# Performance work log

Measured on AMD Instinct MI355X. Metric: run time of the kernel, lower is better.

## Reference

```python
import jax, jax.numpy as jnp
import numpy as np

EPS = 1e-5
NUM_GROUPS = 32
MIN_POINTS = 4

def group_norm(x, gamma, beta):
    # x: [N, C]; torch GroupNorm applied on (1, C, N): normalize each group over (C/G, N)
    N, C = x.shape
    xg = x.reshape(N, NUM_GROUPS, C // NUM_GROUPS)
    mean = jnp.mean(xg, axis=(0, 2), keepdims=True)
    var = jnp.mean((xg - mean) ** 2, axis=(0, 2), keepdims=True)
    xn = (xg - mean) * jax.lax.rsqrt(var + EPS)
    return xn.reshape(N, C) * gamma + beta

def setup_inputs() -> dict:
    key = jax.random.key(0)
    ks = jax.random.split(key, 12)
    N, V = 1000000, 100000
    C0, C = 3, 64  # input feats (minus barycentric col), hidden width
    distributed = jax.random.normal(ks[0], (N, C0 + 1), dtype=jnp.float32)
    indices = jax.random.randint(ks[1], (N,), 0, V, dtype=jnp.int32)
    # kaiming_normal fan_in, relu: std = sqrt(2 / fan_in)
    W0 = jax.random.normal(ks[2], (C, C0), dtype=jnp.float32) * np.sqrt(2.0 / C0)
    W1 = jax.random.normal(ks[3], (C, C), dtype=jnp.float32) * np.sqrt(2.0 / C)
    W2 = jax.random.normal(ks[4], (C, C), dtype=jnp.float32) * np.sqrt(2.0 / C)
    b2 = jnp.zeros((C,), dtype=jnp.float32)
    g0 = jnp.ones((C,), dtype=jnp.float32)
    beta0 = jnp.zeros((C,), dtype=jnp.float32)
    g1 = jnp.ones((C,), dtype=jnp.float32)
    beta1 = jnp.zeros((C,), dtype=jnp.float32)
    return {"distributed": distributed, "indices": indices, "num_vertices": V,
            "W0": W0, "W1": W1, "W2": W2, "b2": b2,
            "g0": g0, "beta0": beta0, "g1": g1, "beta1": beta1}

def reference(distributed, indices, num_vertices, W0, W1, W2, b2, g0, beta0, g1, beta1):
    N = distributed.shape[0]
    V = int(num_vertices)
    bary = distributed[:, -1]            # [N]
    x = distributed[:, :-1]              # [N, C0]
    # layer 0: linear (no bias) -> GN -> relu
    x = jax.nn.relu(group_norm(x @ W0.T, g0, beta0))
    # layer 1: linear (no bias) -> GN -> relu
    x = jax.nn.relu(group_norm(x @ W1.T, g1, beta1))
    # layer 2 (last): linear with bias -> relu (no norm)
    x = jax.nn.relu(x @ W2.T + b2)       # [N, C]
    idx = jnp.maximum(indices.astype(jnp.int32), 0)
    # scatter-max pooling into lattice vertices
    seg_max = jax.ops.segment_max(x, idx, num_segments=V)          # [V, C], -inf for empty
    seg_max = jnp.where(jnp.isneginf(seg_max), 0.0, seg_max)
    counts = jax.ops.segment_sum(jnp.ones((N,), x.dtype), idx, num_segments=V)  # [V]
    # argmax recovery: first point index attaining the per-segment max, per channel
    gathered_max = seg_max[idx]                                    # [N, C]
    cand = jnp.where(x == gathered_max, jnp.arange(N, dtype=jnp.int32)[:, None], N)
    argmax = jax.ops.segment_min(cand, idx, num_segments=V)        # [V, C]
    argmax = jnp.minimum(argmax, N - 1)
    bary_reduced = bary[argmax]                                    # [V, C]
    out = jnp.concatenate([seg_max, bary_reduced], axis=1)         # [V, 2C]
    few = (counts < MIN_POINTS)[:, None]
    return jnp.where(few, 0.0, out)
```

## Files before the change

kernel.cpp:

```cpp
#include <hip/hip_runtime.h>
#include <hip/hip_bf16.h>
#include <math.h>

#define MIN_POINTS 4

#define WS_W0P   0
#define WS_B0P   768
#define WS_W1P   1024
#define WS_B1P   17408
#define WS_CNT   17920
#define WS_P0    417920
#define WS_P1    548992
#define NPART    1024
#define TS       68

__global__ void k_stats0(const float4* __restrict__ d4, const int* __restrict__ idx,
                         double* __restrict__ partial0, int* __restrict__ cnt, int N){
  __shared__ double red[4][16];
  int tid = blockIdx.x*blockDim.x + threadIdx.x;
  int stride = gridDim.x*blockDim.x;
  double a[9] = {0,0,0,0,0,0,0,0,0};
  for (int i = tid; i < N; i += stride){
    float4 d = d4[i];
    double x0 = d.x, x1 = d.y, x2 = d.z;
    a[0] += x0; a[1] += x1; a[2] += x2;
    a[3] = fma(x0,x0,a[3]); a[4] = fma(x0,x1,a[4]); a[5] = fma(x0,x2,a[5]);
    a[6] = fma(x1,x1,a[6]); a[7] = fma(x1,x2,a[7]); a[8] = fma(x2,x2,a[8]);
    int v = idx[i]; if (v < 0) v = 0;
    atomicAdd(&cnt[v], 1);
  }
  int lane = threadIdx.x & 63, wid = threadIdx.x >> 6;
  #pragma unroll
  for (int j = 0; j < 9; j++){
    double v = a[j];
    for (int o = 32; o > 0; o >>= 1) v += __shfl_down(v, o, 64);
    if (lane == 0) red[wid][j] = v;
  }
  __syncthreads();
  if (threadIdx.x < 9){
    double s = red[0][threadIdx.x] + red[1][threadIdx.x]
             + red[2][threadIdx.x] + red[3][threadIdx.x];
    partial0[blockIdx.x*16 + threadIdx.x] = s;
  }
}

__global__ void k_fold0(const double* __restrict__ partial0, const float* __restrict__ W0,
                        const float* __restrict__ g0, const float* __restrict__ bt0,
                        float* __restrict__ w0p, float* __restrict__ b0p, int N, int nparts){
  __shared__ double sred[16];
  int t = threadIdx.x, lane = t & 63, g = t >> 6;
  if (g < 9){
    double s = 0.0;
    for (int b = lane; b < nparts; b += 64) s += partial0[b*16 + g];
    for (int o = 32; o > 0; o >>= 1) s += __shfl_down(s, o, 64);
    if (lane == 0) sred[g] = s;
  }
  __syncthreads();
  if (t < 64){
    int c = t;
    double sx0 = sred[0], sx1 = sred[1], sx2 = sred[2];
    double G00 = sred[3], G01 = sred[4], G02 = sred[5], G11 = sred[6], G12 = sred[7], G22 = sred[8];
    double s[2], q[2];
    int chans[2] = { c, c ^ 1 };
    #pragma unroll
    for (int u = 0; u < 2; u++){
      int ch = chans[u];
      double w0 = W0[ch*3+0], w1 = W0[ch*3+1], w2 = W0[ch*3+2];
      s[u] = w0*sx0 + w1*sx1 + w2*sx2;
      q[u] = w0*w0*G00 + w1*w1*G11 + w2*w2*G22 + 2.0*(w0*w1*G01 + w0*w2*G02 + w1*w2*G12);
    }
    double inv  = 1.0 / (2.0 * (double)N);
    double mean = (s[0] + s[1]) * inv;
    double var  = (q[0] + q[1]) * inv - mean*mean;
    double aa   = (1.0 / sqrt(var + 1e-5)) * (double)g0[c];
    b0p[c] = (float)((double)bt0[c] - mean * aa);
    w0p[c]       = (float)((double)W0[c*3+0] * aa);
    w0p[64 + c]  = (float)((double)W0[c*3+1] * aa);
    w0p[128 + c] = (float)((double)W0[c*3+2] * aa);
  }
}

__global__ __launch_bounds__(256, 4)
void k_stats1(const float4* __restrict__ d4,
              const float* __restrict__ w0p, const float* __restrict__ b0p,
              const float* __restrict__ W1, double* __restrict__ part1,
              int N, int ntiles){
  __shared__ float stage[64][TS];
  __shared__ double red[4][128];
  int lane = threadIdx.x & 63;
  int wid  = __builtin_amdgcn_readfirstlane((int)(threadIdx.x >> 6));
  int cbase = wid * 16;
  float w1r[64];
  #pragma unroll
  for (int k = 0; k < 64; k += 4){
    float4 t = *(const float4*)&W1[lane*64 + k];
    w1r[k]=t.x; w1r[k+1]=t.y; w1r[k+2]=t.z; w1r[k+3]=t.w;
  }
  double s0 = 0.0, s1 = 0.0;
  for (int t = blockIdx.x; t < ntiles; t += gridDim.x){
    int rb = t * 64;
    int row = rb + lane;
    float4 d = (row < N) ? d4[row] : make_float4(0.f,0.f,0.f,0.f);
    #pragma unroll
    for (int g = 0; g < 4; g++){
      int c = cbase + g*4;
      float4 h;
      h.x = fmaxf(fmaf(w0p[128+c+0], d.z, fmaf(w0p[64+c+0], d.y, fmaf(w0p[c+0], d.x, b0p[c+0]))), 0.f);
      h.y = fmaxf(fmaf(w0p[128+c+1], d.z, fmaf(w0p[64+c+1], d.y, fmaf(w0p[c+1], d.x, b0p[c+1]))), 0.f);
      h.z = fmaxf(fmaf(w0p[128+c+2], d.z, fmaf(w0p[64+c+2], d.y, fmaf(w0p[c+2], d.x, b0p[c+2]))), 0.f);
      h.w = fmaxf(fmaf(w0p[128+c+3], d.z, fmaf(w0p[64+c+3], d.y, fmaf(w0p[c+3], d.x, b0p[c+3]))), 0.f);
      *(float4*)&stage[lane][c] = h;
    }
    __syncthreads();
    #pragma unroll 2
    for (int rr = 0; rr < 16; rr++){
      int r = cbase + rr;
      float a0 = 0.f, a1 = 0.f, a2 = 0.f, a3 = 0.f;
      #pragma unroll
      for (int kb = 0; kb < 16; kb++){
        float4 h = *(const float4*)&stage[r][kb*4];
        a0 = fmaf(w1r[kb*4+0], h.x, a0);
        a1 = fmaf(w1r[kb*4+1], h.y, a1);
        a2 = fmaf(w1r[kb*4+2], h.z, a2);
        a3 = fmaf(w1r[kb*4+3], h.w, a3);
      }
      if (rb + r < N){
        double y = (double)((a0 + a1) + (a2 + a3));
        s0 += y;
        s1 = fma(y, y, s1);
      }
    }
    __syncthreads();
  }
  red[wid][lane]      = s0;
  red[wid][64 + lane] = s1;
  __syncthreads();
  if (threadIdx.x < 128){
    int t = threadIdx.x;
    part1[blockIdx.x*128 + t] = red[0][t] + red[1][t] + red[2][t] + red[3][t];
  }
}

__global__ void k_fold1(const double* __restrict__ part1, const float* __restrict__ W1,
                        const float* __restrict__ g1, const float* __restrict__ bt1,
                        float* __restrict__ w1p, float* __restrict__ b1p, int N, int nparts){
  __shared__ double sst[128];
  int t = threadIdx.x;
  int s = t >> 3, j = t & 7;
  double acc = 0.0;
  for (int b = j; b < nparts; b += 8) acc += part1[b*128 + s];
  acc += __shfl_down(acc, 4, 8);
  acc += __shfl_down(acc, 2, 8);
  acc += __shfl_down(acc, 1, 8);
  if (j == 0) sst[s] = acc;
  __syncthreads();
  if (t < 64){
    int c = t, p = c ^ 1;
    double inv  = 1.0 / (2.0 * (double)N);
    double mean = (sst[c] + sst[p]) * inv;
    double Ey2  = (sst[64+c] + sst[64+p]) * inv;
    double var  = Ey2 - mean*mean;
    double a    = (1.0 / sqrt(var + 1e-5)) * (double)g1[c];
    b1p[c] = (float)((double)bt1[c] - mean * a);
    for (int k = 0; k < 64; k++)
      w1p[c*64 + k] = (float)((double)W1[c*64 + k] * a);
  }
}

__global__ __launch_bounds__(64, 2)
void k_main(const float4* __restrict__ d4, const int* __restrict__ idx,
            const float* __restrict__ w0p, const float* __restrict__ b0p,
            const float* __restrict__ w1p, const float* __restrict__ b1p,
            const float* __restrict__ W2,  const float* __restrict__ b2,
            unsigned long long* __restrict__ seg, int N, int ntiles){
  __shared__ float xch[64][65];
  int lane = threadIdx.x;
  for (int t = blockIdx.x; t < ntiles; t += gridDim.x){
    int rb  = t * 64;
    int row = rb + lane;
    float4 d = (row < N) ? d4[row] : make_float4(0.f,0.f,0.f,0.f);
    int myv = 0;
    if (row < N){ int v = idx[row]; myv = (v < 0) ? 0 : v; }
    float h0[64];
    #pragma unroll
    for (int c = 0; c < 64; c++){
      float t0 = fmaf(w0p[128+c], d.z, fmaf(w0p[64+c], d.y, fmaf(w0p[c], d.x, b0p[c])));
      h0[c] = fmaxf(t0, 0.f);
    }
    for (int c = 0; c < 64; c++){
      const float* wr = &w1p[c*64];
      float a0 = b1p[c], a1 = 0.f, a2 = 0.f, a3 = 0.f;
      #pragma unroll
      for (int k = 0; k < 64; k += 4){
        a0 = fmaf(wr[k+0], h0[k+0], a0);
        a1 = fmaf(wr[k+1], h0[k+1], a1);
        a2 = fmaf(wr[k+2], h0[k+2], a2);
        a3 = fmaf(wr[k+3], h0[k+3], a3);
      }
      xch[lane][c] = fmaxf((a0 + a1) + (a2 + a3), 0.f);
    }
    __syncthreads();
    float h1[64];
    #pragma unroll
    for (int k = 0; k < 64; k++) h1[k] = xch[lane][k];
    __syncthreads();
    for (int c = 0; c < 64; c++){
      const float* wr = &W2[c*64];
      float a0 = b2[c], a1 = 0.f, a2 = 0.f, a3 = 0.f;
      #pragma unroll
      for (int k = 0; k < 64; k += 4){
        a0 = fmaf(wr[k+0], h1[k+0], a0);
        a1 = fmaf(wr[k+1], h1[k+1], a1);
        a2 = fmaf(wr[k+2], h1[k+2], a2);
        a3 = fmaf(wr[k+3], h1[k+3], a3);
      }
      xch[lane][c] = fmaxf((a0 + a1) + (a2 + a3), 0.f);
    }
    __syncthreads();
    int rmax = min(64, N - rb);
    for (int r = 0; r < rmax; r++){
      float y = xch[r][lane];
      int v = __builtin_amdgcn_readlane(myv, r);
      unsigned int bits = __float_as_uint(y) & 0x7fffffffu;
      unsigned long long packed = ((unsigned long long)bits << 32)
          | (unsigned long long)(unsigned int)(~(unsigned int)(rb + r));
      atomicMax(&seg[(size_t)v*64 + lane], packed);
    }
    __syncthreads();
  }
}

__global__ void k_out(const float4* __restrict__ d4, const int* __restrict__ cnt,
                      float* __restrict__ out, int N, int V){
  int lane = threadIdx.x & 63;
  int w = (int)((blockIdx.x*blockDim.x + threadIdx.x) >> 6);
  if (w >= V) return;
  const unsigned long long* seg = (const unsigned long long*)out;
  unsigned long long p = seg[(size_t)w*64 + lane];
  int c = cnt[w];
  unsigned int bits = (unsigned int)(p >> 32);
  unsigned int rowu = ~(unsigned int)p;
  unsigned int nm1 = (unsigned int)(N - 1);
  if (rowu > nm1) rowu = nm1;
  float val  = __uint_as_float(bits);
  float bary = d4[rowu].w;
  bool few = (c < MIN_POINTS);
  float o0 = few ? 0.f : val;
  float o1 = few ? 0.f : bary;
  out[(size_t)w*128 + lane]      = o0;
  out[(size_t)w*128 + 64 + lane] = o1;
}

extern "C" void kernel_launch(void* const* d_in, const int* in_sizes, int n_in,
                              void* d_out, int out_size, void* d_ws, size_t ws_size,
                              hipStream_t stream) {
  const float4* d4  = (const float4*)d_in[0];
  const int*    idx = (const int*)d_in[1];
  const float*  W0  = (const float*)d_in[3];
  const float*  W1  = (const float*)d_in[4];
  const float*  W2  = (const float*)d_in[5];
  const float*  b2  = (const float*)d_in[6];
  const float*  g0  = (const float*)d_in[7];
  const float*  bt0 = (const float*)d_in[8];
  const float*  g1  = (const float*)d_in[9];
  const float*  bt1 = (const float*)d_in[10];

  int N = in_sizes[0] / 4;
  int V = out_size / 128;
  int ntiles = (N + 63) / 64;

  char* ws = (char*)d_ws;
  float*  w0p = (float*)(ws + WS_W0P);
  float*  b0p = (float*)(ws + WS_B0P);
  float*  w1p = (float*)(ws + WS_W1P);
  float*  b1p = (float*)(ws + WS_B1P);
  int*    cnt = (int*)(ws + WS_CNT);
  double* p0  = (double*)(ws + WS_P0);
  double* p1  = (double*)(ws + WS_P1);

  hipMemsetAsync(cnt, 0, (size_t)V * sizeof(int), stream);
  hipMemsetAsync(d_out, 0, (size_t)out_size * sizeof(float), stream);

  k_stats0<<<NPART, 256, 0, stream>>>(d4, idx, p0, cnt, N);
  k_fold0 <<<1, 1024, 0, stream>>>(p0, W0, g0, bt0, w0p, b0p, N, NPART);
  k_stats1<<<NPART, 256, 0, stream>>>(d4, w0p, b0p, W1, p1, N, ntiles);
  k_fold1 <<<1, 1024, 0, stream>>>(p1, W1, g1, bt1, w1p, b1p, N, NPART);
  k_main  <<<2048, 64, 0, stream>>>(d4, idx, w0p, b0p, w1p, b1p, W2, b2,
                                    (unsigned long long*)d_out, N, ntiles);
  k_out   <<<(V + 3) / 4, 256, 0, stream>>>(d4, cnt, (float*)d_out, N, V);
}
```

Measured before the change: 815.2 us.

## Halve k_main LDS staging buffer and raise occupancy with chunked scatter

Replaces the 64x65 LDS exchange tile with a 64x33 buffer. Layer-1 outputs are staged in two 32-column halves, and layer-2 outputs are computed and scattered in two 32-channel chunks, with half-waves covering different rows during the atomicMax scatter. Launch bounds go to 4 waves per SIMD and the grid doubles to 4096 blocks. The aim is higher occupancy to hide global and atomic latency, at the cost of tighter register budgets (h0 and h1 arrays) that may spill.

```diff
diff --git a/kernel.cpp b/kernel.cpp
--- a/kernel.cpp
+++ b/kernel.cpp
@@ -167,13 +167,13 @@
   }
 }
 
-__global__ __launch_bounds__(64, 2)
+__global__ __launch_bounds__(64, 4)
 void k_main(const float4* __restrict__ d4, const int* __restrict__ idx,
             const float* __restrict__ w0p, const float* __restrict__ b0p,
             const float* __restrict__ w1p, const float* __restrict__ b1p,
             const float* __restrict__ W2,  const float* __restrict__ b2,
             unsigned long long* __restrict__ seg, int N, int ntiles){
-  __shared__ float xch[64][65];
+  __shared__ float buf[64][33];
   int lane = threadIdx.x;
   for (int t = blockIdx.x; t < ntiles; t += gridDim.x){
     int rb  = t * 64;
@@ -187,7 +187,8 @@
       float t0 = fmaf(w0p[128+c], d.z, fmaf(w0p[64+c], d.y, fmaf(w0p[c], d.x, b0p[c])));
       h0[c] = fmaxf(t0, 0.f);
     }
-    for (int c = 0; c < 64; c++){
+    float h1[64];
+    for (int c = 0; c < 32; c++){
       const float* wr = &w1p[c*64];
       float a0 = b1p[c], a1 = 0.f, a2 = 0.f, a3 = 0.f;
       #pragma unroll
@@ -197,36 +198,57 @@
         a2 = fmaf(wr[k+2], h0[k+2], a2);
         a3 = fmaf(wr[k+3], h0[k+3], a3);
       }
-      xch[lane][c] = fmaxf((a0 + a1) + (a2 + a3), 0.f);
-    }
-    __syncthreads();
-    float h1[64];
-    #pragma unroll
-    for (int k = 0; k < 64; k++) h1[k] = xch[lane][k];
-    __syncthreads();
-    for (int c = 0; c < 64; c++){
-      const float* wr = &W2[c*64];
-      float a0 = b2[c], a1 = 0.f, a2 = 0.f, a3 = 0.f;
+      buf[lane][c] = fmaxf((a0 + a1) + (a2 + a3), 0.f);
+    }
+    #pragma unroll
+    for (int k = 0; k < 32; k++) h1[k] = buf[lane][k];
+    for (int c = 32; c < 64; c++){
+      const float* wr = &w1p[c*64];
+      float a0 = b1p[c], a1 = 0.f, a2 = 0.f, a3 = 0.f;
       #pragma unroll
       for (int k = 0; k < 64; k += 4){
-        a0 = fmaf(wr[k+0], h1[k+0], a0);
-        a1 = fmaf(wr[k+1], h1[k+1], a1);
-        a2 = fmaf(wr[k+2], h1[k+2], a2);
-        a3 = fmaf(wr[k+3], h1[k+3], a3);
-      }
-      xch[lane][c] = fmaxf((a0 + a1) + (a2 + a3), 0.f);
-    }
-    __syncthreads();
-    int rmax = min(64, N - rb);
-    for (int r = 0; r < rmax; r++){
-      float y = xch[r][lane];
-      int v = __builtin_amdgcn_readlane(myv, r);
-      unsigned int bits = __float_as_uint(y) & 0x7fffffffu;
-      unsigned long long packed = ((unsigned long long)bits << 32)
-          | (unsigned long long)(unsigned int)(~(unsigned int)(rb + r));
-      atomicMax(&seg[(size_t)v*64 + lane], packed);
-    }
-    __syncthreads();
+        a0 = fmaf(wr[k+0], h0[k+0], a0);
+        a1 = fmaf(wr[k+1], h0[k+1], a1);
+        a2 = fmaf(wr[k+2], h0[k+2], a2);
+        a3 = fmaf(wr[k+3], h0[k+3], a3);
+      }
+      buf[lane][c - 32] = fmaxf((a0 + a1) + (a2 + a3), 0.f);
+    }
+    #pragma unroll
+    for (int k = 0; k < 32; k++) h1[32 + k] = buf[lane][k];
+    #pragma unroll 1
+    for (int ci = 0; ci < 2; ci++){
+      int cb = ci * 32;
+      for (int cc = 0; cc < 32; cc++){
+        int c = cb + cc;
+        const float* wr = &W2[c*64];
+        float a0 = b2[c], a1 = 0.f, a2 = 0.f, a3 = 0.f;
+        #pragma unroll
+        for (int k = 0; k < 64; k += 4){
+          a0 = fmaf(wr[k+0], h1[k+0], a0);
+          a1 = fmaf(wr[k+1], h1[k+1], a1);
+          a2 = fmaf(wr[k+2], h1[k+2], a2);
+          a3 = fmaf(wr[k+3], h1[k+3], a3);
+        }
+        buf[lane][cc] = fmaxf((a0 + a1) + (a2 + a3), 0.f);
+      }
+      __syncthreads();
+      int jj = lane & 31;
+      for (int rr = 0; rr < 32; rr++){
+        int vA = __builtin_amdgcn_readlane(myv, rr);
+        int vB = __builtin_amdgcn_readlane(myv, rr + 32);
+        int r  = (lane < 32) ? rr : rr + 32;
+        int v  = (lane < 32) ? vA : vB;
+        float y = buf[r][jj];
+        if (rb + r < N){
+          unsigned int bits = __float_as_uint(y) & 0x7fffffffu;
+          unsigned long long packed = ((unsigned long long)bits << 32)
+              | (unsigned long long)(unsigned int)(~(unsigned int)(rb + r));
+          atomicMax(&seg[(size_t)v*64 + cb + jj], packed);
+        }
+      }
+      __syncthreads();
+    }
   }
 }
 
@@ -285,7 +307,7 @@
   k_fold0 <<<1, 1024, 0, stream>>>(p0, W0, g0, bt0, w0p, b0p, N, NPART);
   k_stats1<<<NPART, 256, 0, stream>>>(d4, w0p, b0p, W1, p1, N, ntiles);
   k_fold1 <<<1, 1024, 0, stream>>>(p1, W1, g1, bt1, w1p, b1p, N, NPART);
-  k_main  <<<2048, 64, 0, stream>>>(d4, idx, w0p, b0p, w1p, b1p, W2, b2,
+  k_main  <<<4096, 64, 0, stream>>>(d4, idx, w0p, b0p, w1p, b1p, W2, b2,
                                     (unsigned long long*)d_out, N, ntiles);
   k_out   <<<(V + 3) / 4, 256, 0, stream>>>(d4, cnt, (float*)d_out, N, V);
 }
```

New measurement: 1.671 ms. 2.05x slower.
